# Optimization experiments

Measured on AMD Instinct MI355X. Metric: run time of the kernel, lower is better.

## Reference

```python
import jax, jax.numpy as jnp
import numpy as np

N_HEAD = 16
THETA = 10000.0


def _freqs_cos_sin(head_dim, seq_len):
    # matches precompute_freqs_cis: freqs = 1/theta^(arange(0,dim,2)/dim), outer with t
    inv = 1.0 / (THETA ** (jnp.arange(0, head_dim, 2, dtype=jnp.float32) / head_dim))
    t = jnp.arange(seq_len, dtype=jnp.float32)
    ang = jnp.outer(t, inv)  # [L, head_dim//2]
    return jnp.cos(ang), jnp.sin(ang)


def _rope(x, cos, sin):
    # x: [B, H, L, D]; pairs are interleaved (view_as_complex on (..., D//2, 2))
    x1 = x[..., 0::2]
    x2 = x[..., 1::2]
    out_re = x1 * cos - x2 * sin
    out_im = x1 * sin + x2 * cos
    return jnp.stack([out_re, out_im], axis=-1).reshape(x.shape)


def setup_inputs() -> dict:
    key = jax.random.key(0)
    ks = jax.random.split(key, 11)
    B, L, D = 2, 2048, 1024
    s = 0.02
    return {
        "q": jax.random.normal(ks[0], (B, L, D), jnp.float32),
        "k": jax.random.normal(ks[1], (B, L, D), jnp.float32),
        "v": jax.random.normal(ks[2], (B, L, D), jnp.float32),
        "wq": jax.random.normal(ks[3], (D, D), jnp.float32) * s,
        "bq": jax.random.normal(ks[4], (D,), jnp.float32) * s,
        "wk": jax.random.normal(ks[5], (D, D), jnp.float32) * s,
        "bk": jax.random.normal(ks[6], (D,), jnp.float32) * s,
        "wv": jax.random.normal(ks[7], (D, D), jnp.float32) * s,
        "bv": jax.random.normal(ks[8], (D,), jnp.float32) * s,
        "wo": jax.random.normal(ks[9], (D, D), jnp.float32) * s,
        "bo": jax.random.normal(ks[10], (D,), jnp.float32) * s,
    }


def reference(q, k, v, wq, bq, wk, bk, wv, bv, wo, bo):
    B, L, D = q.shape
    Hd = D // N_HEAD
    # projections (nn.Linear: x @ W^T + b)
    qp = q @ wq.T + bq
    kp = k @ wk.T + bk
    vp = v @ wv.T + bv
    # split: [B, L, D] -> [B, H, L, Hd]
    def split(t):
        return t.reshape(B, L, N_HEAD, Hd).transpose(0, 2, 1, 3)
    qh, kh, vh = split(qp), split(kp), split(vp)
    cos, sin = _freqs_cos_sin(Hd, L)  # [L, Hd//2], broadcasts over B, H
    qh = _rope(qh, cos, sin)
    kh = _rope(kh, cos, sin)
    # scaled dot-product attention (no mask)
    scores = jnp.einsum("bhqd,bhkd->bhqk", qh, kh) / jnp.sqrt(jnp.float32(Hd))
    attn = jax.nn.softmax(scores, axis=-1)
    out = jnp.einsum("bhqk,bhkd->bhqd", attn, vh)
    # concat heads and output projection
    out = out.transpose(0, 2, 1, 3).reshape(B, L, D)
    return out @ wo.T + bo
```

## Files before the change

kernel.cpp:

```cpp
#include <hip/hip_runtime.h>
#include <hip/hip_bf16.h>
#include <math.h>

#define BB 2
#define LL 2048
#define DD 1024
#define NH 16
#define HD 64

typedef short v8s __attribute__((ext_vector_type(8)));
typedef float v4f __attribute__((ext_vector_type(4)));
typedef float v16f __attribute__((ext_vector_type(16)));

__device__ __forceinline__ float b2f(unsigned short b) {
  union { unsigned int u; float f; } c; c.u = ((unsigned int)b) << 16; return c.f;
}
__device__ __forceinline__ unsigned short f2b(float x) {
  union { float f; unsigned int u; } c; c.f = x;
  unsigned int u = c.u;
  u += 0x7fffu + ((u >> 16) & 1u);
  return (unsigned short)(u >> 16);
}
__device__ __forceinline__ unsigned int asu(float x) {
  union { float f; unsigned int u; } c; c.f = x; return c.u;
}
__device__ __forceinline__ unsigned int pk2(float lo, float hi) {
  return __builtin_amdgcn_perm(asu(hi), asu(lo), 0x07060302u);
}

__device__ __forceinline__ void gload16(const void* g, void* l) {
  __builtin_amdgcn_global_load_lds(
      (const __attribute__((address_space(1))) void*)g,
      (__attribute__((address_space(3))) void*)l, 16, 0, 0);
}

struct CastArgs { const float* s[7]; unsigned short* d[7]; };
__global__ void cast_all(CastArgs a) {
  int z = blockIdx.z;
  int t = (z < 12) ? (z >> 2) : (z - 9);
  int off = (z < 12) ? ((z & 3) << 18) : 0;
  int i = off + blockIdx.x * blockDim.x + threadIdx.x;
  float4 v = ((const float4*)a.s[t])[i];
  ushort4 o;
  o.x = f2b(v.x); o.y = f2b(v.y); o.z = f2b(v.z); o.w = f2b(v.w);
  ((ushort4*)a.d[t])[i] = o;
}

__global__ void freqs_kernel(float* __restrict__ ctab, float* __restrict__ stab) {
  int id = blockIdx.x * blockDim.x + threadIdx.x;
  int t = id >> 5, i = id & 31;
  float inv = powf(10000.0f, -(float)(2 * i) / 64.0f);
  float ang = (float)t * inv;
  ctab[id] = cosf(ang);
  stab[id] = sinf(ang);
}

template <typename OutT>
__device__ __forceinline__ void gemm_body(const unsigned short* __restrict__ X,
                                          const unsigned short* __restrict__ W,
                                          const float* __restrict__ bias,
                                          OutT* __restrict__ Y,
                                          int M, int N, int K) {
  __shared__ __align__(16) unsigned short As[128 * 32];
  __shared__ __align__(16) unsigned short Bs[128 * 32];
  const int tid = threadIdx.x;
  const int lane = tid & 63, wave = tid >> 6;
  const int quad = lane >> 4, l16 = lane & 15;
  const int bn0 = blockIdx.x * 128;
  const int bm0 = blockIdx.y * 128;
  const int wm = (wave >> 1) * 64, wn = (wave & 1) * 64;

  const v4f vzero = {0.f, 0.f, 0.f, 0.f};
  v4f acc[4][4];
#pragma unroll
  for (int i = 0; i < 4; ++i)
#pragma unroll
    for (int j = 0; j < 4; ++j) acc[i][j] = vzero;

  const int id0 = tid, id1 = tid + 256;
  const int r0 = id0 >> 2, r1 = id1 >> 2;
  const int c0 = ((id0 & 3) ^ (r0 & 3) ^ ((r0 >> 2) & 3)) * 8;
  const int c1 = ((id1 & 3) ^ (r1 & 3) ^ ((r1 >> 2) & 3)) * 8;

  for (int k0 = 0; k0 < K; k0 += 32) {
    gload16(X + (size_t)(bm0 + r0) * K + k0 + c0, &As[id0 * 8]);
    gload16(X + (size_t)(bm0 + r1) * K + k0 + c1, &As[id1 * 8]);
    gload16(W + (size_t)(bn0 + r0) * K + k0 + c0, &Bs[id0 * 8]);
    gload16(W + (size_t)(bn0 + r1) * K + k0 + c1, &Bs[id1 * 8]);
    __syncthreads();
    v8s a[4], b[4];
#pragma unroll
    for (int i = 0; i < 4; ++i) {
      int ra = wm + i * 16 + l16;
      int ca = quad ^ (ra & 3) ^ ((ra >> 2) & 3);
      a[i] = *(const v8s*)&As[ra * 32 + ca * 8];
      int rb = wn + i * 16 + l16;
      int cb = quad ^ (rb & 3) ^ ((rb >> 2) & 3);
      b[i] = *(const v8s*)&Bs[rb * 32 + cb * 8];
    }
#pragma unroll
    for (int mi = 0; mi < 4; ++mi)
#pragma unroll
      for (int ni = 0; ni < 4; ++ni)
        acc[mi][ni] = __builtin_amdgcn_mfma_f32_16x16x32_bf16(a[mi], b[ni], acc[mi][ni], 0, 0, 0);
    __syncthreads();
  }

  float bv[4];
#pragma unroll
  for (int ni = 0; ni < 4; ++ni) bv[ni] = bias[bn0 + wn + ni * 16 + l16];
#pragma unroll
  for (int mi = 0; mi < 4; ++mi) {
#pragma unroll
    for (int r = 0; r < 4; ++r) {
      int row = bm0 + wm + mi * 16 + quad * 4 + r;
      size_t base = (size_t)row * N + bn0 + wn + l16;
#pragma unroll
      for (int ni = 0; ni < 4; ++ni) {
        float v = acc[mi][ni][r] + bv[ni];
        if constexpr (sizeof(OutT) == 2) {
          Y[base + ni * 16] = (OutT)f2b(v);
        } else {
          Y[base + ni * 16] = (OutT)v;
        }
      }
    }
  }
}

__global__ __launch_bounds__(256) void gemm_qkv(
    const unsigned short* x0, const unsigned short* w0, const float* b0, unsigned short* y0,
    const unsigned short* x1, const unsigned short* w1, const float* b1, unsigned short* y1,
    const unsigned short* x2, const unsigned short* w2, const float* b2, unsigned short* y2) {
  const unsigned short *X, *W; const float* Bp; unsigned short* Y;
  if (blockIdx.z == 0)      { X = x0; W = w0; Bp = b0; Y = y0; }
  else if (blockIdx.z == 1) { X = x1; W = w1; Bp = b1; Y = y1; }
  else                      { X = x2; W = w2; Bp = b2; Y = y2; }
  gemm_body<unsigned short>(X, W, Bp, Y, BB * LL, DD, DD);
}

__global__ __launch_bounds__(256) void gemm_out(
    const unsigned short* x, const unsigned short* w, const float* b, float* y) {
  gemm_body<float>(x, w, b, y, BB * LL, DD, DD);
}

__global__ void rope_kernel(const unsigned short* __restrict__ qp,
                            const unsigned short* __restrict__ kp,
                            unsigned short* __restrict__ qh,
                            unsigned short* __restrict__ kh,
                            const float* __restrict__ ctab,
                            const float* __restrict__ stab) {
  int id = blockIdx.x * blockDim.x + threadIdx.x;
  const unsigned short* src = (blockIdx.z == 0) ? qp : kp;
  unsigned short* dst = (blockIdx.z == 0) ? qh : kh;
  float sc = (blockIdx.z == 0) ? 0.125f : 1.0f;
  int i = id & 31;
  int l = (id >> 5) & (LL - 1);
  int h = (id >> 16) & (NH - 1);
  int b = id >> 20;
  ushort2 v = ((const ushort2*)(src + ((size_t)(b * LL + l) * DD + h * HD)))[i];
  float c = ctab[l * 32 + i], s = stab[l * 32 + i];
  float x1 = b2f(v.x), x2 = b2f(v.y);
  ushort2 o;
  o.x = f2b((x1 * c - x2 * s) * sc);
  o.y = f2b((x1 * s + x2 * c) * sc);
  ((ushort2*)(dst + (size_t)((b * NH + h) * LL + l) * HD))[i] = o;
}

__global__ void vtrans_kernel(const unsigned short* __restrict__ vp,
                              unsigned short* __restrict__ vt) {
  __shared__ unsigned short T[64][65];
  int bh = blockIdx.y;
  int b = bh >> 4, h = bh & 15;
  int l0 = blockIdx.x * 64;
  int t = threadIdx.x;
  int lr = t >> 2, seg = (t & 3) * 16;
  const unsigned short* src = vp + ((size_t)(b * LL + l0 + lr) * DD + h * HD + seg);
  ushort4 u0 = ((const ushort4*)src)[0];
  ushort4 u1 = ((const ushort4*)src)[1];
  ushort4 u2 = ((const ushort4*)src)[2];
  ushort4 u3 = ((const ushort4*)src)[3];
  T[lr][seg + 0] = u0.x;  T[lr][seg + 1] = u0.y;  T[lr][seg + 2] = u0.z;  T[lr][seg + 3] = u0.w;
  T[lr][seg + 4] = u1.x;  T[lr][seg + 5] = u1.y;  T[lr][seg + 6] = u1.z;  T[lr][seg + 7] = u1.w;
  T[lr][seg + 8] = u2.x;  T[lr][seg + 9] = u2.y;  T[lr][seg + 10] = u2.z; T[lr][seg + 11] = u2.w;
  T[lr][seg + 12] = u3.x; T[lr][seg + 13] = u3.y; T[lr][seg + 14] = u3.z; T[lr][seg + 15] = u3.w;
  __syncthreads();
  int dr = t >> 2, ls = (t & 3) * 16;
  unsigned short* dst = vt + ((size_t)(bh * HD + dr) * LL + l0 + ls);
  ushort4 o0, o1, o2, o3;
  o0.x = T[ls + 0][dr];  o0.y = T[ls + 1][dr];  o0.z = T[ls + 2][dr];  o0.w = T[ls + 3][dr];
  o1.x = T[ls + 4][dr];  o1.y = T[ls + 5][dr];  o1.z = T[ls + 6][dr];  o1.w = T[ls + 7][dr];
  o2.x = T[ls + 8][dr];  o2.y = T[ls + 9][dr];  o2.z = T[ls + 10][dr]; o2.w = T[ls + 11][dr];
  o3.x = T[ls + 12][dr]; o3.y = T[ls + 13][dr]; o3.z = T[ls + 14][dr]; o3.w = T[ls + 15][dr];
  ((ushort4*)dst)[0] = o0; ((ushort4*)dst)[2] = o1;
  ((ushort4*)dst)[1] = o2; ((ushort4*)dst)[3] = o3;
}

__global__ __launch_bounds__(256) void flash_kernel(
    const unsigned short* __restrict__ qh,
    const unsigned short* __restrict__ kh,
    const unsigned short* __restrict__ vt,
    unsigned short* __restrict__ attn) {
  __shared__ __align__(16) unsigned short Ks[128 * 64];
  __shared__ __align__(16) unsigned short Vs[64 * 128];
  const int tid = threadIdx.x, wave = tid >> 6, lane = tid & 63;
  const int l32 = lane & 31, hf = lane >> 5;
  const int bh = blockIdx.y, b = bh >> 4, hd = bh & 15;
  const int q0 = blockIdx.x * 128;
  const unsigned short* qbase = qh + (size_t)bh * LL * HD;
  const unsigned short* kbase = kh + (size_t)bh * LL * HD;
  const unsigned short* vbase = vt + (size_t)bh * HD * LL;

  const int qrow = q0 + wave * 32 + l32;
  v8s qf[4];
#pragma unroll
  for (int ks2 = 0; ks2 < 4; ++ks2)
    qf[ks2] = *(const v8s*)(qbase + (size_t)qrow * HD + ks2 * 16 + hf * 8);

  v16f o0, o1;
#pragma unroll
  for (int i = 0; i < 16; ++i) { o0[i] = 0.0f; o1[i] = 0.0f; }
  float ls = 0.0f;

  for (int kt = 0; kt < LL; kt += 128) {
#pragma unroll
    for (int i = 0; i < 4; ++i) {
      int id = i * 256 + tid;
      int r = id >> 3, c = (id & 7) ^ (r & 7);
      gload16(kbase + (size_t)(kt + r) * HD + c * 8, &Ks[id * 8]);
    }
#pragma unroll
    for (int i = 0; i < 4; ++i) {
      int id = i * 256 + tid;
      int r = id >> 4, c = (id & 15) ^ (r & 15);
      gload16(vbase + (size_t)r * LL + kt + c * 8, &Vs[id * 8]);
    }
    __syncthreads();

#pragma unroll
    for (int g = 0; g < 4; ++g) {
      v16f sc;
#pragma unroll
      for (int i = 0; i < 16; ++i) sc[i] = 0.0f;
#pragma unroll
      for (int ks2 = 0; ks2 < 4; ++ks2) {
        int row = g * 32 + l32;
        int slot = (ks2 * 2 + hf) ^ (lane & 7);
        v8s kf = *(const v8s*)&Ks[row * 64 + slot * 8];
        sc = __builtin_amdgcn_mfma_f32_32x32x16_bf16(kf, qf[ks2], sc, 0, 0, 0);
      }
      v16f e;
#pragma unroll
      for (int i = 0; i < 16; ++i) e[i] = __expf(sc[i]);
      float t0 = (e[0] + e[1]) + (e[2] + e[3]);
      float t1 = (e[4] + e[5]) + (e[6] + e[7]);
      float t2 = (e[8] + e[9]) + (e[10] + e[11]);
      float t3 = (e[12] + e[13]) + (e[14] + e[15]);
      ls += (t0 + t1) + (t2 + t3);
#pragma unroll
      for (int k2 = 0; k2 < 2; ++k2) {
        union { v8s v; unsigned int u[4]; } pb;
#pragma unroll
        for (int a = 0; a < 4; ++a)
          pb.u[a] = pk2(e[8 * k2 + 2 * a], e[8 * k2 + 2 * a + 1]);
        int k16 = g * 2 + k2;
        {
          int slotv = (k16 * 2 + hf) ^ (lane & 15);
          v8s vf = *(const v8s*)&Vs[l32 * 128 + slotv * 8];
          o0 = __builtin_amdgcn_mfma_f32_32x32x16_bf16(vf, pb.v, o0, 0, 0, 0);
        }
        {
          int slotv = (k16 * 2 + hf) ^ (lane & 15);
          v8s vf = *(const v8s*)&Vs[(32 + l32) * 128 + slotv * 8];
          o1 = __builtin_amdgcn_mfma_f32_32x32x16_bf16(vf, pb.v, o1, 0, 0, 0);
        }
      }
    }
    __syncthreads();
  }

  ls += __shfl_xor(ls, 32);
  float inv = 1.0f / ls;

  unsigned short* Wt = &Ks[wave * 2048];
#pragma unroll
  for (int dt = 0; dt < 2; ++dt)
#pragma unroll
    for (int r = 0; r < 16; ++r) {
      int dl = (r & 3) + 8 * (r >> 2) + 4 * hf;
      int d = dt * 32 + dl;
      int chunk = d >> 3, offw = d & 7;
      int slot = chunk ^ (l32 & 7);
      float val = (dt == 0) ? o0[r] : o1[r];
      Wt[l32 * 64 + slot * 8 + offw] = f2b(val * inv);
    }
#pragma unroll
  for (int i = 0; i < 4; ++i) {
    int qr = lane >> 1;
    int chunk = (lane & 1) * 4 + i;
    int slot = chunk ^ (qr & 7);
    v8s dv = *(const v8s*)&Wt[qr * 64 + slot * 8];
    int token = q0 + wave * 32 + qr;
    *(v8s*)(attn + ((size_t)(b * LL + token) * DD) + hd * HD + chunk * 8) = dv;
  }
}

extern "C" void kernel_launch(void* const* d_in, const int* in_sizes, int n_in,
                              void* d_out, int out_size, void* d_ws, size_t ws_size,
                              hipStream_t stream) {
  const float* q  = (const float*)d_in[0];
  const float* k  = (const float*)d_in[1];
  const float* v  = (const float*)d_in[2];
  const float* wq = (const float*)d_in[3];
  const float* bq = (const float*)d_in[4];
  const float* wk = (const float*)d_in[5];
  const float* bk = (const float*)d_in[6];
  const float* wv = (const float*)d_in[7];
  const float* bv = (const float*)d_in[8];
  const float* wo = (const float*)d_in[9];
  const float* bo = (const float*)d_in[10];
  float* out = (float*)d_out;

  size_t off = 0;
  char* wsb = (char*)d_ws;
  auto take = [&](size_t n) { void* p = wsb + off; off += n; return p; };
  const size_t SZT = (size_t)BB * LL * DD * 2;
  const size_t SZW = (size_t)DD * DD * 2;
  unsigned short* qb   = (unsigned short*)take(SZT);
  unsigned short* kb   = (unsigned short*)take(SZT);
  unsigned short* vb   = (unsigned short*)take(SZT);
  unsigned short* wqb  = (unsigned short*)take(SZW);
  unsigned short* wkb  = (unsigned short*)take(SZW);
  unsigned short* wvb  = (unsigned short*)take(SZW);
  unsigned short* wob  = (unsigned short*)take(SZW);
  unsigned short* qp   = (unsigned short*)take(SZT);
  unsigned short* kp   = (unsigned short*)take(SZT);
  unsigned short* vp   = (unsigned short*)take(SZT);
  unsigned short* qhh  = (unsigned short*)take(SZT);
  unsigned short* khh  = (unsigned short*)take(SZT);
  unsigned short* vtt  = (unsigned short*)take(SZT);
  unsigned short* attn = (unsigned short*)take(SZT);
  float* ctab = (float*)take((size_t)LL * 32 * 4);
  float* stab = (float*)take((size_t)LL * 32 * 4);

  CastArgs ca;
  ca.s[0] = q;  ca.s[1] = k;  ca.s[2] = v;  ca.s[3] = wq;
  ca.s[4] = wk; ca.s[5] = wv; ca.s[6] = wo;
  ca.d[0] = qb;  ca.d[1] = kb;  ca.d[2] = vb;  ca.d[3] = wqb;
  ca.d[4] = wkb; ca.d[5] = wvb; ca.d[6] = wob;
  cast_all<<<dim3(1024, 1, 16), 256, 0, stream>>>(ca);
  freqs_kernel<<<(LL * 32) / 256, 256, 0, stream>>>(ctab, stab);

  gemm_qkv<<<dim3(DD / 128, BB * LL / 128, 3), 256, 0, stream>>>(
      qb, wqb, bq, qp, kb, wkb, bk, kp, vb, wvb, bv, vp);

  rope_kernel<<<dim3((BB * NH * LL * 32) / 256, 1, 2), 256, 0, stream>>>(
      qp, kp, qhh, khh, ctab, stab);
  vtrans_kernel<<<dim3(LL / 64, BB * NH), 256, 0, stream>>>(vp, vtt);

  flash_kernel<<<dim3(LL / 128, BB * NH), 256, 0, stream>>>(qhh, khh, vtt, attn);

  gemm_out<<<dim3(DD / 128, BB * LL / 128, 1), 256, 0, stream>>>(attn, wob, bo, out);
}
```

Baseline: 243.6 us.

## Fuse RoPE into QKV GEMM epilogue and split attention over two KV halves

The QKV projection kernel now applies RoPE and the query scaling in its epilogue, swapping pair values with a lane shuffle and writing head-major Q/K directly. This removes the separate rope kernel and its round trip through global memory. Flash attention is split into two KV halves along a new grid dimension, which doubles the block count for better CU utilisation. Each half writes unnormalised bf16 partial outputs and row sums, and a new reduce kernel combines them into the head-concatenated layout. The cost is an extra kernel launch, more partial-buffer traffic, bf16 rounding of the unnormalised partials, and partial buffers that reuse workspace holding the already-consumed input casts.

```diff
diff --git a/kernel.cpp b/kernel.cpp
--- a/kernel.cpp
+++ b/kernel.cpp
@@ -129,42 +129,106 @@
 }
 
 __global__ __launch_bounds__(256) void gemm_qkv(
-    const unsigned short* x0, const unsigned short* w0, const float* b0, unsigned short* y0,
-    const unsigned short* x1, const unsigned short* w1, const float* b1, unsigned short* y1,
-    const unsigned short* x2, const unsigned short* w2, const float* b2, unsigned short* y2) {
-  const unsigned short *X, *W; const float* Bp; unsigned short* Y;
-  if (blockIdx.z == 0)      { X = x0; W = w0; Bp = b0; Y = y0; }
-  else if (blockIdx.z == 1) { X = x1; W = w1; Bp = b1; Y = y1; }
-  else                      { X = x2; W = w2; Bp = b2; Y = y2; }
-  gemm_body<unsigned short>(X, W, Bp, Y, BB * LL, DD, DD);
+    const unsigned short* __restrict__ qb, const unsigned short* __restrict__ kb,
+    const unsigned short* __restrict__ vb,
+    const unsigned short* __restrict__ wqb, const unsigned short* __restrict__ wkb,
+    const unsigned short* __restrict__ wvb,
+    const float* __restrict__ bq, const float* __restrict__ bk,
+    const float* __restrict__ bv_,
+    unsigned short* __restrict__ qhh, unsigned short* __restrict__ khh,
+    unsigned short* __restrict__ vp,
+    const float* __restrict__ ctab, const float* __restrict__ stab) {
+  __shared__ __align__(16) unsigned short As[128 * 32];
+  __shared__ __align__(16) unsigned short Bs[128 * 32];
+  const int z = blockIdx.z;
+  const unsigned short* X = (z == 0) ? qb : (z == 1) ? kb : vb;
+  const unsigned short* W = (z == 0) ? wqb : (z == 1) ? wkb : wvb;
+  const float* bias = (z == 0) ? bq : (z == 1) ? bk : bv_;
+  const int K = DD, N = DD;
+  const int tid = threadIdx.x;
+  const int lane = tid & 63, wave = tid >> 6;
+  const int quad = lane >> 4, l16 = lane & 15;
+  const int bn0 = blockIdx.x * 128;
+  const int bm0 = blockIdx.y * 128;
+  const int wm = (wave >> 1) * 64, wn = (wave & 1) * 64;
+
+  const v4f vzero = {0.f, 0.f, 0.f, 0.f};
+  v4f acc[4][4];
+#pragma unroll
+  for (int i = 0; i < 4; ++i)
+#pragma unroll
+    for (int j = 0; j < 4; ++j) acc[i][j] = vzero;
+
+  const int id0 = tid, id1 = tid + 256;
+  const int r0 = id0 >> 2, r1 = id1 >> 2;
+  const int c0 = ((id0 & 3) ^ (r0 & 3) ^ ((r0 >> 2) & 3)) * 8;
+  const int c1 = ((id1 & 3) ^ (r1 & 3) ^ ((r1 >> 2) & 3)) * 8;
+
+  for (int k0 = 0; k0 < K; k0 += 32) {
+    gload16(X + (size_t)(bm0 + r0) * K + k0 + c0, &As[id0 * 8]);
+    gload16(X + (size_t)(bm0 + r1) * K + k0 + c1, &As[id1 * 8]);
+    gload16(W + (size_t)(bn0 + r0) * K + k0 + c0, &Bs[id0 * 8]);
+    gload16(W + (size_t)(bn0 + r1) * K + k0 + c1, &Bs[id1 * 8]);
+    __syncthreads();
+    v8s a[4], b[4];
+#pragma unroll
+    for (int i = 0; i < 4; ++i) {
+      int ra = wm + i * 16 + l16;
+      int ca = quad ^ (ra & 3) ^ ((ra >> 2) & 3);
+      a[i] = *(const v8s*)&As[ra * 32 + ca * 8];
+      int rb = wn + i * 16 + l16;
+      int cb = quad ^ (rb & 3) ^ ((rb >> 2) & 3);
+      b[i] = *(const v8s*)&Bs[rb * 32 + cb * 8];
+    }
+#pragma unroll
+    for (int mi = 0; mi < 4; ++mi)
+#pragma unroll
+      for (int ni = 0; ni < 4; ++ni)
+        acc[mi][ni] = __builtin_amdgcn_mfma_f32_16x16x32_bf16(a[mi], b[ni], acc[mi][ni], 0, 0, 0);
+    __syncthreads();
+  }
+
+  float bv[4];
+#pragma unroll
+  for (int ni = 0; ni < 4; ++ni) bv[ni] = bias[bn0 + wn + ni * 16 + l16];
+
+  if (z == 2) {
+#pragma unroll
+    for (int mi = 0; mi < 4; ++mi)
+#pragma unroll
+      for (int r = 0; r < 4; ++r) {
+        int row = bm0 + wm + mi * 16 + quad * 4 + r;
+        size_t base = (size_t)row * N + bn0 + wn + l16;
+#pragma unroll
+        for (int ni = 0; ni < 4; ++ni)
+          vp[base + ni * 16] = f2b(acc[mi][ni][r] + bv[ni]);
+      }
+  } else {
+    unsigned short* dst = (z == 0) ? qhh : khh;
+    const float scq = (z == 0) ? 0.125f : 1.0f;
+#pragma unroll
+    for (int mi = 0; mi < 4; ++mi)
+#pragma unroll
+      for (int r = 0; r < 4; ++r) {
+        int row = bm0 + wm + mi * 16 + quad * 4 + r;
+        int bb_ = row >> 11, l = row & (LL - 1);
+#pragma unroll
+        for (int ni = 0; ni < 4; ++ni) {
+          float v = acc[mi][ni][r] + bv[ni];
+          float p = __shfl_xor(v, 1);
+          int f = bn0 + wn + ni * 16 + l16;
+          int ii = (f >> 1) & 31;
+          float c = ctab[l * 32 + ii], s = stab[l * 32 + ii];
+          float o = ((f & 1) ? (p * s + v * c) : (v * c - p * s)) * scq;
+          dst[((size_t)(bb_ * NH + (f >> 6)) * LL + l) * HD + (f & 63)] = f2b(o);
+        }
+      }
+  }
 }
 
 __global__ __launch_bounds__(256) void gemm_out(
     const unsigned short* x, const unsigned short* w, const float* b, float* y) {
   gemm_body<float>(x, w, b, y, BB * LL, DD, DD);
-}
-
-__global__ void rope_kernel(const unsigned short* __restrict__ qp,
-                            const unsigned short* __restrict__ kp,
-                            unsigned short* __restrict__ qh,
-                            unsigned short* __restrict__ kh,
-                            const float* __restrict__ ctab,
-                            const float* __restrict__ stab) {
-  int id = blockIdx.x * blockDim.x + threadIdx.x;
-  const unsigned short* src = (blockIdx.z == 0) ? qp : kp;
-  unsigned short* dst = (blockIdx.z == 0) ? qh : kh;
-  float sc = (blockIdx.z == 0) ? 0.125f : 1.0f;
-  int i = id & 31;
-  int l = (id >> 5) & (LL - 1);
-  int h = (id >> 16) & (NH - 1);
-  int b = id >> 20;
-  ushort2 v = ((const ushort2*)(src + ((size_t)(b * LL + l) * DD + h * HD)))[i];
-  float c = ctab[l * 32 + i], s = stab[l * 32 + i];
-  float x1 = b2f(v.x), x2 = b2f(v.y);
-  ushort2 o;
-  o.x = f2b((x1 * c - x2 * s) * sc);
-  o.y = f2b((x1 * s + x2 * c) * sc);
-  ((ushort2*)(dst + (size_t)((b * NH + h) * LL + l) * HD))[i] = o;
 }
 
 __global__ void vtrans_kernel(const unsigned short* __restrict__ vp,
@@ -196,16 +260,17 @@
   ((ushort4*)dst)[1] = o2; ((ushort4*)dst)[3] = o3;
 }
 
-__global__ __launch_bounds__(256) void flash_kernel(
+__global__ __launch_bounds__(256, 4) void flash_kernel(
     const unsigned short* __restrict__ qh,
     const unsigned short* __restrict__ kh,
     const unsigned short* __restrict__ vt,
-    unsigned short* __restrict__ attn) {
+    unsigned short* __restrict__ po, float* __restrict__ pl) {
   __shared__ __align__(16) unsigned short Ks[128 * 64];
   __shared__ __align__(16) unsigned short Vs[64 * 128];
   const int tid = threadIdx.x, wave = tid >> 6, lane = tid & 63;
   const int l32 = lane & 31, hf = lane >> 5;
-  const int bh = blockIdx.y, b = bh >> 4, hd = bh & 15;
+  const int bh = blockIdx.y;
+  const int split = blockIdx.z;
   const int q0 = blockIdx.x * 128;
   const unsigned short* qbase = qh + (size_t)bh * LL * HD;
   const unsigned short* kbase = kh + (size_t)bh * LL * HD;
@@ -222,7 +287,8 @@
   for (int i = 0; i < 16; ++i) { o0[i] = 0.0f; o1[i] = 0.0f; }
   float ls = 0.0f;
 
-  for (int kt = 0; kt < LL; kt += 128) {
+  const int kt0 = split * (LL / 2);
+  for (int kt = kt0; kt < kt0 + LL / 2; kt += 128) {
 #pragma unroll
     for (int i = 0; i < 4; ++i) {
       int id = i * 256 + tid;
@@ -280,7 +346,7 @@
   }
 
   ls += __shfl_xor(ls, 32);
-  float inv = 1.0f / ls;
+  if (hf == 0) pl[((size_t)split * 32 + bh) * LL + q0 + wave * 32 + l32] = ls;
 
   unsigned short* Wt = &Ks[wave * 2048];
 #pragma unroll
@@ -292,7 +358,7 @@
       int chunk = d >> 3, offw = d & 7;
       int slot = chunk ^ (l32 & 7);
       float val = (dt == 0) ? o0[r] : o1[r];
-      Wt[l32 * 64 + slot * 8 + offw] = f2b(val * inv);
+      Wt[l32 * 64 + slot * 8 + offw] = f2b(val);
     }
 #pragma unroll
   for (int i = 0; i < 4; ++i) {
@@ -301,8 +367,25 @@
     int slot = chunk ^ (qr & 7);
     v8s dv = *(const v8s*)&Wt[qr * 64 + slot * 8];
     int token = q0 + wave * 32 + qr;
-    *(v8s*)(attn + ((size_t)(b * LL + token) * DD) + hd * HD + chunk * 8) = dv;
-  }
+    *(v8s*)(po + (((size_t)split * 32 + bh) * LL + token) * HD + chunk * 8) = dv;
+  }
+}
+
+__global__ void reduce_kernel(const unsigned short* __restrict__ po,
+                              const float* __restrict__ pl,
+                              unsigned short* __restrict__ attn) {
+  int id = blockIdx.x * blockDim.x + threadIdx.x;
+  int dg = id & 7, q = (id >> 3) & (LL - 1), bh = id >> 14;
+  int b = bh >> 4, h = bh & 15;
+  size_t base = ((size_t)bh * LL + q) * HD + dg * 8;
+  v8s a = *(const v8s*)(po + base);
+  v8s c = *(const v8s*)(po + base + (size_t)32 * LL * HD);
+  float inv = 1.0f / (pl[bh * LL + q] + pl[(32 + bh) * LL + q]);
+  v8s o;
+#pragma unroll
+  for (int j = 0; j < 8; ++j)
+    o[j] = (short)f2b((b2f((unsigned short)a[j]) + b2f((unsigned short)c[j])) * inv);
+  *(v8s*)(attn + ((size_t)(b * LL + q) * DD) + h * HD + dg * 8) = o;
 }
 
 extern "C" void kernel_launch(void* const* d_in, const int* in_sizes, int n_in,
@@ -333,15 +416,15 @@
   unsigned short* wkb  = (unsigned short*)take(SZW);
   unsigned short* wvb  = (unsigned short*)take(SZW);
   unsigned short* wob  = (unsigned short*)take(SZW);
-  unsigned short* qp   = (unsigned short*)take(SZT);
-  unsigned short* kp   = (unsigned short*)take(SZT);
-  unsigned short* vp   = (unsigned short*)take(SZT);
   unsigned short* qhh  = (unsigned short*)take(SZT);
   unsigned short* khh  = (unsigned short*)take(SZT);
+  unsigned short* vp   = (unsigned short*)take(SZT);
   unsigned short* vtt  = (unsigned short*)take(SZT);
   unsigned short* attn = (unsigned short*)take(SZT);
   float* ctab = (float*)take((size_t)LL * 32 * 4);
   float* stab = (float*)take((size_t)LL * 32 * 4);
+  unsigned short* po = (unsigned short*)wsb;
+  float* pl = (float*)(wsb + ((size_t)16 << 20));
 
   CastArgs ca;
   ca.s[0] = q;  ca.s[1] = k;  ca.s[2] = v;  ca.s[3] = wq;
@@ -352,13 +435,12 @@
   freqs_kernel<<<(LL * 32) / 256, 256, 0, stream>>>(ctab, stab);
 
   gemm_qkv<<<dim3(DD / 128, BB * LL / 128, 3), 256, 0, stream>>>(
-      qb, wqb, bq, qp, kb, wkb, bk, kp, vb, wvb, bv, vp);
-
-  rope_kernel<<<dim3((BB * NH * LL * 32) / 256, 1, 2), 256, 0, stream>>>(
-      qp, kp, qhh, khh, ctab, stab);
+      qb, kb, vb, wqb, wkb, wvb, bq, bk, bv, qhh, khh, vp, ctab, stab);
+
   vtrans_kernel<<<dim3(LL / 64, BB * NH), 256, 0, stream>>>(vp, vtt);
 
-  flash_kernel<<<dim3(LL / 128, BB * NH), 256, 0, stream>>>(qhh, khh, vtt, attn);
+  flash_kernel<<<dim3(LL / 128, BB * NH, 2), 256, 0, stream>>>(qhh, khh, vtt, po, pl);
+  reduce_kernel<<<(32 * LL * 8) / 256, 256, 0, stream>>>(po, pl, attn);
 
   gemm_out<<<dim3(DD / 128, BB * LL / 128, 1), 256, 0, stream>>>(attn, wob, bo, out);
 }
```

Result: slower. 258.2 us (+6.0%).

## Split flash attention over two KV halves with reduce kernel; widen GEMM K tile

Applied to the files above, without the earlier changes.

The flash kernel now splits the key/value sequence into two halves along a third grid dimension. This doubles the number of blocks so more of the GPU's compute units have work. Each half writes unnormalized partial outputs in bf16 plus its row sums, and a new reduce kernel adds them, normalizes and scatters the result into the head-interleaved layout. The projection GEMM also moves from a K step of 32 to 64 with an 8-way XOR swizzle, halving the barrier count per tile. In exchange it adds an extra kernel launch, a partial-output round trip through memory that reuses dead workspace, and bf16 rounding of the partials before they are combined.

```diff
diff --git a/kernel.cpp b/kernel.cpp
--- a/kernel.cpp
+++ b/kernel.cpp
@@ -61,8 +61,8 @@
                                           const float* __restrict__ bias,
                                           OutT* __restrict__ Y,
                                           int M, int N, int K) {
-  __shared__ __align__(16) unsigned short As[128 * 32];
-  __shared__ __align__(16) unsigned short Bs[128 * 32];
+  __shared__ __align__(16) unsigned short As[128 * 64];
+  __shared__ __align__(16) unsigned short Bs[128 * 64];
   const int tid = threadIdx.x;
   const int lane = tid & 63, wave = tid >> 6;
   const int quad = lane >> 4, l16 = lane & 15;
@@ -77,32 +77,38 @@
 #pragma unroll
     for (int j = 0; j < 4; ++j) acc[i][j] = vzero;
 
-  const int id0 = tid, id1 = tid + 256;
-  const int r0 = id0 >> 2, r1 = id1 >> 2;
-  const int c0 = ((id0 & 3) ^ (r0 & 3) ^ ((r0 >> 2) & 3)) * 8;
-  const int c1 = ((id1 & 3) ^ (r1 & 3) ^ ((r1 >> 2) & 3)) * 8;
-
-  for (int k0 = 0; k0 < K; k0 += 32) {
-    gload16(X + (size_t)(bm0 + r0) * K + k0 + c0, &As[id0 * 8]);
-    gload16(X + (size_t)(bm0 + r1) * K + k0 + c1, &As[id1 * 8]);
-    gload16(W + (size_t)(bn0 + r0) * K + k0 + c0, &Bs[id0 * 8]);
-    gload16(W + (size_t)(bn0 + r1) * K + k0 + c1, &Bs[id1 * 8]);
+  for (int k0 = 0; k0 < K; k0 += 64) {
+#pragma unroll
+    for (int c = 0; c < 4; ++c) {
+      int id = c * 256 + tid;
+      int r = id >> 3, cc = ((id & 7) ^ (r & 7)) * 8;
+      gload16(X + (size_t)(bm0 + r) * K + k0 + cc, &As[id * 8]);
+    }
+#pragma unroll
+    for (int c = 0; c < 4; ++c) {
+      int id = c * 256 + tid;
+      int r = id >> 3, cc = ((id & 7) ^ (r & 7)) * 8;
+      gload16(W + (size_t)(bn0 + r) * K + k0 + cc, &Bs[id * 8]);
+    }
     __syncthreads();
-    v8s a[4], b[4];
-#pragma unroll
-    for (int i = 0; i < 4; ++i) {
-      int ra = wm + i * 16 + l16;
-      int ca = quad ^ (ra & 3) ^ ((ra >> 2) & 3);
-      a[i] = *(const v8s*)&As[ra * 32 + ca * 8];
-      int rb = wn + i * 16 + l16;
-      int cb = quad ^ (rb & 3) ^ ((rb >> 2) & 3);
-      b[i] = *(const v8s*)&Bs[rb * 32 + cb * 8];
-    }
-#pragma unroll
-    for (int mi = 0; mi < 4; ++mi)
-#pragma unroll
-      for (int ni = 0; ni < 4; ++ni)
-        acc[mi][ni] = __builtin_amdgcn_mfma_f32_16x16x32_bf16(a[mi], b[ni], acc[mi][ni], 0, 0, 0);
+#pragma unroll
+    for (int kh = 0; kh < 2; ++kh) {
+      v8s a[4], b[4];
+#pragma unroll
+      for (int i = 0; i < 4; ++i) {
+        int ra = wm + i * 16 + l16;
+        int sa = (kh * 4 + quad) ^ (ra & 7);
+        a[i] = *(const v8s*)&As[ra * 64 + sa * 8];
+        int rb = wn + i * 16 + l16;
+        int sb = (kh * 4 + quad) ^ (rb & 7);
+        b[i] = *(const v8s*)&Bs[rb * 64 + sb * 8];
+      }
+#pragma unroll
+      for (int mi = 0; mi < 4; ++mi)
+#pragma unroll
+        for (int ni = 0; ni < 4; ++ni)
+          acc[mi][ni] = __builtin_amdgcn_mfma_f32_16x16x32_bf16(a[mi], b[ni], acc[mi][ni], 0, 0, 0);
+    }
     __syncthreads();
   }
 
@@ -196,16 +202,17 @@
   ((ushort4*)dst)[1] = o2; ((ushort4*)dst)[3] = o3;
 }
 
-__global__ __launch_bounds__(256) void flash_kernel(
+__global__ __launch_bounds__(256, 4) void flash_kernel(
     const unsigned short* __restrict__ qh,
     const unsigned short* __restrict__ kh,
     const unsigned short* __restrict__ vt,
-    unsigned short* __restrict__ attn) {
+    unsigned short* __restrict__ po, float* __restrict__ pl) {
   __shared__ __align__(16) unsigned short Ks[128 * 64];
   __shared__ __align__(16) unsigned short Vs[64 * 128];
   const int tid = threadIdx.x, wave = tid >> 6, lane = tid & 63;
   const int l32 = lane & 31, hf = lane >> 5;
-  const int bh = blockIdx.y, b = bh >> 4, hd = bh & 15;
+  const int bh = blockIdx.y;
+  const int split = blockIdx.z;
   const int q0 = blockIdx.x * 128;
   const unsigned short* qbase = qh + (size_t)bh * LL * HD;
   const unsigned short* kbase = kh + (size_t)bh * LL * HD;
@@ -222,7 +229,8 @@
   for (int i = 0; i < 16; ++i) { o0[i] = 0.0f; o1[i] = 0.0f; }
   float ls = 0.0f;
 
-  for (int kt = 0; kt < LL; kt += 128) {
+  const int kt0 = split * (LL / 2);
+  for (int kt = kt0; kt < kt0 + LL / 2; kt += 128) {
 #pragma unroll
     for (int i = 0; i < 4; ++i) {
       int id = i * 256 + tid;
@@ -280,7 +288,7 @@
   }
 
   ls += __shfl_xor(ls, 32);
-  float inv = 1.0f / ls;
+  if (hf == 0) pl[((size_t)split * 32 + bh) * LL + q0 + wave * 32 + l32] = ls;
 
   unsigned short* Wt = &Ks[wave * 2048];
 #pragma unroll
@@ -292,7 +300,7 @@
       int chunk = d >> 3, offw = d & 7;
       int slot = chunk ^ (l32 & 7);
       float val = (dt == 0) ? o0[r] : o1[r];
-      Wt[l32 * 64 + slot * 8 + offw] = f2b(val * inv);
+      Wt[l32 * 64 + slot * 8 + offw] = f2b(val);
     }
 #pragma unroll
   for (int i = 0; i < 4; ++i) {
@@ -301,8 +309,25 @@
     int slot = chunk ^ (qr & 7);
     v8s dv = *(const v8s*)&Wt[qr * 64 + slot * 8];
     int token = q0 + wave * 32 + qr;
-    *(v8s*)(attn + ((size_t)(b * LL + token) * DD) + hd * HD + chunk * 8) = dv;
+    *(v8s*)(po + (((size_t)split * 32 + bh) * LL + token) * HD + chunk * 8) = dv;
   }
+}
+
+__global__ void reduce_kernel(const unsigned short* __restrict__ po,
+                              const float* __restrict__ pl,
+                              unsigned short* __restrict__ attn) {
+  int id = blockIdx.x * blockDim.x + threadIdx.x;
+  int dg = id & 7, q = (id >> 3) & (LL - 1), bh = id >> 14;
+  int b = bh >> 4, h = bh & 15;
+  size_t base = ((size_t)bh * LL + q) * HD + dg * 8;
+  v8s a = *(const v8s*)(po + base);
+  v8s c = *(const v8s*)(po + base + (size_t)32 * LL * HD);
+  float inv = 1.0f / (pl[bh * LL + q] + pl[(32 + bh) * LL + q]);
+  v8s o;
+#pragma unroll
+  for (int j = 0; j < 8; ++j)
+    o[j] = (short)f2b((b2f((unsigned short)a[j]) + b2f((unsigned short)c[j])) * inv);
+  *(v8s*)(attn + ((size_t)(b * LL + q) * DD) + h * HD + dg * 8) = o;
 }
 
 extern "C" void kernel_launch(void* const* d_in, const int* in_sizes, int n_in,
@@ -342,6 +367,8 @@
   unsigned short* attn = (unsigned short*)take(SZT);
   float* ctab = (float*)take((size_t)LL * 32 * 4);
   float* stab = (float*)take((size_t)LL * 32 * 4);
+  unsigned short* po = (unsigned short*)wsb;
+  float* pl = (float*)(wsb + ((size_t)16 << 20));
 
   CastArgs ca;
   ca.s[0] = q;  ca.s[1] = k;  ca.s[2] = v;  ca.s[3] = wq;
@@ -358,7 +385,8 @@
       qp, kp, qhh, khh, ctab, stab);
   vtrans_kernel<<<dim3(LL / 64, BB * NH), 256, 0, stream>>>(vp, vtt);
 
-  flash_kernel<<<dim3(LL / 128, BB * NH), 256, 0, stream>>>(qhh, khh, vtt, attn);
+  flash_kernel<<<dim3(LL / 128, BB * NH, 2), 256, 0, stream>>>(qhh, khh, vtt, po, pl);
+  reduce_kernel<<<(32 * LL * 8) / 256, 256, 0, stream>>>(po, pl, attn);
 
   gemm_out<<<dim3(DD / 128, BB * LL / 128, 1), 256, 0, stream>>>(attn, wob, bo, out);
 }
```

New measurement: 254.0 us. 4.3% more time.
